# Kernel optimization log

Hardware: AMD Instinct MI355X
Metric: run time of the kernel (lower is better)

The kernel has to match this reference:

```python
import jax, jax.numpy as jnp
import numpy as np

LN_EPS = 1e-5


def _ln(x, g, b):
    mu = jnp.mean(x, -1, keepdims=True)
    xc = x - mu
    inv = jax.lax.rsqrt(jnp.mean(xc * xc, -1, keepdims=True) + LN_EPS)
    return xc * inv * g + b


def _subm_conv(x, nbr, W, b):
    # Submanifold 3D conv via rulebook gather-GEMM-accumulate.
    # x: [N, Cin], nbr: [N, K] neighbor row ids (-1 = missing), W: [K, Cin, Cout], b: [Cout]
    N = x.shape[0]
    xp = jnp.concatenate([x, jnp.zeros((1, x.shape[1]), x.dtype)], 0)  # sentinel zero row
    idx = jnp.where(nbr < 0, N, nbr)  # missing neighbors -> zero row
    acc0 = jnp.zeros((N, W.shape[-1]), x.dtype) + b
    def body(acc, xs):
        i, Wk = xs  # i: [N], Wk: [Cin, Cout]
        return acc + xp[i] @ Wk, None
    acc, _ = jax.lax.scan(body, acc0, (idx.T, W))
    return acc


def _blk1(x, W, b, g, be):  # 1x1x1 SubMConv + LN + ReLU
    return jax.nn.relu(_ln(x @ W + b, g, be))


def _blk3(x, nbr, W, b, g, be):  # 3x3x3 SubMConv + LN + ReLU
    return jax.nn.relu(_ln(_subm_conv(x, nbr, W, b), g, be))


def setup_inputs() -> dict:
    rng = np.random.default_rng(0)
    B, D, Npb, K = 2, 160, 131072, 27
    dim, half = 64, 32
    # Build random sparse voxel set and the rulebook (neighbor table) like spconv does.
    lookup = np.full((B, D, D, D), -1, np.int64)
    coords = np.zeros((B * Npb, 3), np.int64)
    for b in range(B):
        lin = np.sort(rng.choice(D * D * D, size=Npb, replace=False))
        z, y, x = np.unravel_index(lin, (D, D, D))
        rows = np.arange(b * Npb, (b + 1) * Npb)
        lookup[b, z, y, x] = rows
        coords[rows] = np.stack([z, y, x], 1)
    bidx = np.repeat(np.arange(B), Npb)
    offs = np.stack(np.meshgrid(np.arange(-1, 2), np.arange(-1, 2), np.arange(-1, 2), indexing="ij"), -1).reshape(K, 3)
    nz = coords[:, None, :] + offs[None]  # [N, K, 3]
    valid = ((nz >= 0) & (nz < D)).all(-1)
    nzc = np.clip(nz, 0, D - 1)
    nbr = lookup[bidx[:, None], nzc[..., 0], nzc[..., 1], nzc[..., 2]]
    nbr = np.where(valid, nbr, -1).astype(np.int32)

    key = jax.random.key(0)
    ks = iter(jax.random.split(key, 16))
    f32 = jnp.float32
    d = {"voxel_features": jax.random.normal(next(ks), (B * Npb, dim), f32),
         "nbr_idx": jnp.asarray(nbr)}
    def lnp(c):
        return jnp.ones((c,), f32), jnp.zeros((c,), f32)
    d["W1"] = 0.05 * jax.random.normal(next(ks), (dim, dim), f32); d["b1"] = jnp.zeros((dim,), f32); d["g1"], d["be1"] = lnp(dim)
    d["W2"] = 0.05 * jax.random.normal(next(ks), (dim, dim), f32); d["b2"] = jnp.zeros((dim,), f32); d["g2"], d["be2"] = lnp(dim)
    d["W3"] = 0.05 * jax.random.normal(next(ks), (K, dim, half), f32); d["b3"] = jnp.zeros((half,), f32); d["g3"], d["be3"] = lnp(half)
    d["W4"] = 0.05 * jax.random.normal(next(ks), (K, half, half), f32); d["b4"] = jnp.zeros((half,), f32); d["g4"], d["be4"] = lnp(half)
    d["W5"] = 0.05 * jax.random.normal(next(ks), (K, half, half), f32); d["b5"] = jnp.zeros((half,), f32); d["g5"], d["be5"] = lnp(half)
    d["W6"] = 0.05 * jax.random.normal(next(ks), (K, half, half), f32); d["b6"] = jnp.zeros((half,), f32); d["g6"], d["be6"] = lnp(half)
    d["W7"] = 0.05 * jax.random.normal(next(ks), (4 * dim, dim), f32); d["b7"] = jnp.zeros((dim,), f32); d["g7"], d["be7"] = lnp(dim)
    return d


def reference(voxel_features, nbr_idx,
              W1, b1, g1, be1, W2, b2, g2, be2,
              W3, b3, g3, be3, W4, b4, g4, be4,
              W5, b5, g5, be5, W6, b6, g6, be6,
              W7, b7, g7, be7):
    x = voxel_features
    f1 = _blk1(x, W1, b1, g1, be1)
    f2 = _blk1(x, W2, b2, g2, be2)
    feats = [f1, f2]
    f2 = _blk3(f2, nbr_idx, W3, b3, g3, be3); feats.append(f2)
    f2 = _blk3(f2, nbr_idx, W4, b4, g4, be4); feats.append(f2)
    f2 = _blk3(f2, nbr_idx, W5, b5, g5, be5); feats.append(f2)
    f2 = _blk3(f2, nbr_idx, W6, b6, g6, be6); feats.append(f2)
    cat = jnp.concatenate(feats, -1)  # [N, 4*dim]
    return _blk1(cat, W7, b7, g7, be7)
```

## Files before the change

### kernel.cpp

```cpp
#include <hip/hip_runtime.h>

typedef __attribute__((ext_vector_type(4))) float  float4_;
typedef __attribute__((ext_vector_type(8))) short  short8;
typedef __attribute__((ext_vector_type(8))) __bf16 bf16x8;

__device__ inline unsigned short f2bf(float f) {
    unsigned u = __builtin_bit_cast(unsigned, f);
    u += 0x7FFFu + ((u >> 16) & 1u);
    return (unsigned short)(u >> 16);
}

__device__ inline float4_ mfma16(bf16x8 a, bf16x8 b, float4_ c) {
    return __builtin_amdgcn_mfma_f32_16x16x32_bf16(a, b, c, 0, 0, 0);
}

__device__ inline void packW_one(const float* __restrict__ src, unsigned short* __restrict__ dst,
                                 int cin, int cout, int e) {
    int f = e >> 9, i = e & 511, lane = i >> 3, t = i & 7;
    int ntn = cout >> 4, ctn = cin >> 5;
    int nt = f % ntn;
    int rest = f / ntn;
    int ct = rest % ctn;
    int k = rest / ctn;
    int c = ct * 32 + (lane >> 4) * 8 + t;
    int j = nt * 16 + (lane & 15);
    dst[e] = f2bf(src[(k * cin + c) * cout + j]);
}

__global__ void pack_all_kernel(
    const float* __restrict__ W1, const float* __restrict__ W2,
    const float* __restrict__ W3, const float* __restrict__ W4,
    const float* __restrict__ W5, const float* __restrict__ W6,
    const float* __restrict__ W7,
    unsigned short* cat, unsigned short* Wp12, unsigned short* Wp3,
    unsigned short* Wp4, unsigned short* Wp5, unsigned short* Wp6,
    unsigned short* Wp7, int N) {
    int e = blockIdx.x * 256 + threadIdx.x;
    if (e < 8192) {
        int f = e >> 9, i = e & 511, lane = i >> 3, t = i & 7;
        int nt = f & 7, ct = f >> 3;
        int c = ct * 32 + (lane >> 4) * 8 + t;
        int j = nt * 16 + (lane & 15);
        float v = (j < 64) ? W1[c * 64 + j] : W2[c * 64 + (j - 64)];
        Wp12[e] = f2bf(v);
        return;
    }
    e -= 8192;
    if (e < 55296) { packW_one(W3, Wp3, 64, 32, e); return; }
    e -= 55296;
    if (e < 27648) { packW_one(W4, Wp4, 32, 32, e); return; }
    e -= 27648;
    if (e < 27648) { packW_one(W5, Wp5, 32, 32, e); return; }
    e -= 27648;
    if (e < 27648) { packW_one(W6, Wp6, 32, 32, e); return; }
    e -= 27648;
    if (e < 16384) { packW_one(W7, Wp7, 256, 64, e); return; }
    e -= 16384;
    if (e < 128) ((unsigned*)(cat + (size_t)N * 256))[e] = 0;
}

__global__ void nbrT_kernel(const int* __restrict__ nbr, int* __restrict__ nbrT, int N) {
    int row = blockIdx.x * 256 + threadIdx.x;
    if (row >= N) return;
#pragma unroll
    for (int k = 0; k < 27; k++) {
        int v = nbr[(size_t)row * 27 + k];
        nbrT[(size_t)k * N + row] = v < 0 ? N : v;
    }
}

__global__ __launch_bounds__(256) void blk12_kernel(
    const float* __restrict__ x, unsigned short* cat,
    const unsigned short* __restrict__ Wp,
    const float* __restrict__ b1, const float* __restrict__ g1, const float* __restrict__ be1,
    const float* __restrict__ b2, const float* __restrict__ g2, const float* __restrict__ be2) {
    int tid = threadIdx.x, lane = tid & 63, wv = tid >> 6;
    int l15 = lane & 15, q = lane >> 4;
    long base = ((long)blockIdx.x * 4 + wv) * 16;

    float4_ acc[8];
#pragma unroll
    for (int i = 0; i < 8; i++) acc[i] = (float4_){0.f, 0.f, 0.f, 0.f};

#pragma unroll
    for (int kt = 0; kt < 2; kt++) {
        const float* xp = x + (base + l15) * 64 + kt * 32 + q * 8;
        float4_ f0 = *(const float4_*)xp;
        float4_ f1 = *(const float4_*)(xp + 4);
        short8 as;
        as[0] = (short)f2bf(f0[0]); as[1] = (short)f2bf(f0[1]);
        as[2] = (short)f2bf(f0[2]); as[3] = (short)f2bf(f0[3]);
        as[4] = (short)f2bf(f1[0]); as[5] = (short)f2bf(f1[1]);
        as[6] = (short)f2bf(f1[2]); as[7] = (short)f2bf(f1[3]);
        bf16x8 a = __builtin_bit_cast(bf16x8, as);
        const unsigned short* wp = Wp + (size_t)kt * 8 * 512;
#pragma unroll
        for (int nt = 0; nt < 8; nt++) {
            bf16x8 w = *(const bf16x8*)(wp + nt * 512 + lane * 8);
            acc[nt] = mfma16(a, w, acc[nt]);
        }
    }

    float bc[8], gc[8], bec[8];
#pragma unroll
    for (int nt = 0; nt < 8; nt++) {
        int j = nt * 16 + l15;
        if (j < 64) { bc[nt] = b1[j]; gc[nt] = g1[j]; bec[nt] = be1[j]; }
        else        { bc[nt] = b2[j - 64]; gc[nt] = g2[j - 64]; bec[nt] = be2[j - 64]; }
    }

#pragma unroll
    for (int r = 0; r < 4; r++) {
        long row = base + q * 4 + r;
        float v[8], s0 = 0.f, s1 = 0.f, q0 = 0.f, q1 = 0.f;
#pragma unroll
        for (int nt = 0; nt < 4; nt++) { v[nt] = acc[nt][r] + bc[nt]; s0 += v[nt]; q0 += v[nt] * v[nt]; }
#pragma unroll
        for (int nt = 4; nt < 8; nt++) { v[nt] = acc[nt][r] + bc[nt]; s1 += v[nt]; q1 += v[nt] * v[nt]; }
#pragma unroll
        for (int m = 1; m < 16; m <<= 1) {
            s0 += __shfl_xor(s0, m); q0 += __shfl_xor(q0, m);
            s1 += __shfl_xor(s1, m); q1 += __shfl_xor(q1, m);
        }
        float mu0 = s0 * (1.f / 64), var0 = q0 * (1.f / 64) - mu0 * mu0, inv0 = rsqrtf(var0 + 1e-5f);
        float mu1 = s1 * (1.f / 64), var1 = q1 * (1.f / 64) - mu1 * mu1, inv1 = rsqrtf(var1 + 1e-5f);
        unsigned short* cp = cat + row * 256;
#pragma unroll
        for (int nt = 0; nt < 4; nt++) {
            float y = fmaxf((v[nt] - mu0) * inv0 * gc[nt] + bec[nt], 0.f);
            cp[nt * 16 + l15] = f2bf(y);
        }
#pragma unroll
        for (int nt = 4; nt < 8; nt++) {
            float y = fmaxf((v[nt] - mu1) * inv1 * gc[nt] + bec[nt], 0.f);
            cp[nt * 16 + l15] = f2bf(y);
        }
    }
}

template <int CT, int D>
__global__ __launch_bounds__(256) void conv_kernel(
    unsigned short* cat, const int* __restrict__ nbrT,
    const unsigned short* __restrict__ Wp,
    const float* __restrict__ bb, const float* __restrict__ gg, const float* __restrict__ bee,
    int in_off, int out_off, int N) {
    const int MT = 2;
    int tid = threadIdx.x, lane = tid & 63, wv = tid >> 6;
    int l15 = lane & 15, q = lane >> 4;
    int G = gridDim.x;
    int eff = (blockIdx.x & 7) * (G >> 3) + (blockIdx.x >> 3);
    long base = ((long)eff * 4 + wv) * 32;

    float4_ acc[MT][2];
#pragma unroll
    for (int mt = 0; mt < MT; mt++) {
        acc[mt][0] = (float4_){0.f, 0.f, 0.f, 0.f};
        acc[mt][1] = (float4_){0.f, 0.f, 0.f, 0.f};
    }

    const unsigned short* catp = cat + in_off + q * 8;
    const unsigned short* wl = Wp + lane * 8;
    long r0 = base + l15, r1 = base + 16 + l15;

    int    idxr[D + 1][MT];
    bf16x8 f[D + 1][MT][CT];
    bf16x8 wr[D + 1][CT][2];

#pragma unroll
    for (int j = 0; j < D; j++) {
        idxr[j][0] = nbrT[(size_t)j * N + r0];
        idxr[j][1] = nbrT[(size_t)j * N + r1];
    }
#pragma unroll
    for (int j = 0; j < D; j++) {
#pragma unroll
        for (int mt = 0; mt < MT; mt++) {
            size_t s = (size_t)idxr[j % (D + 1)][mt];
#pragma unroll
            for (int ct = 0; ct < CT; ct++)
                f[j % (D + 1)][mt][ct] = *(const bf16x8*)(catp + s * 256 + ct * 32);
        }
#pragma unroll
        for (int ct = 0; ct < CT; ct++)
#pragma unroll
            for (int nt = 0; nt < 2; nt++)
                wr[j % (D + 1)][ct][nt] =
                    *(const bf16x8*)(wl + ((size_t)((j * CT + ct) * 2 + nt)) * 512);
        if (j + D < 27) {
            idxr[(j + D) % (D + 1)][0] = nbrT[(size_t)(j + D) * N + r0];
            idxr[(j + D) % (D + 1)][1] = nbrT[(size_t)(j + D) * N + r1];
        }
    }

#pragma unroll
    for (int k = 0; k < 27; k++) {
        if (k + D < 27) {
#pragma unroll
            for (int mt = 0; mt < MT; mt++) {
                size_t s = (size_t)idxr[(k + D) % (D + 1)][mt];
#pragma unroll
                for (int ct = 0; ct < CT; ct++)
                    f[(k + D) % (D + 1)][mt][ct] = *(const bf16x8*)(catp + s * 256 + ct * 32);
            }
#pragma unroll
            for (int ct = 0; ct < CT; ct++)
#pragma unroll
                for (int nt = 0; nt < 2; nt++)
                    wr[(k + D) % (D + 1)][ct][nt] =
                        *(const bf16x8*)(wl + ((size_t)(((k + D) * CT + ct) * 2 + nt)) * 512);
        }
        if (k + 2 * D < 27) {
            idxr[(k + 2 * D) % (D + 1)][0] = nbrT[(size_t)(k + 2 * D) * N + r0];
            idxr[(k + 2 * D) % (D + 1)][1] = nbrT[(size_t)(k + 2 * D) * N + r1];
        }
        __builtin_amdgcn_sched_barrier(0);
#pragma unroll
        for (int ct = 0; ct < CT; ct++) {
            bf16x8 w0 = wr[k % (D + 1)][ct][0];
            bf16x8 w1 = wr[k % (D + 1)][ct][1];
#pragma unroll
            for (int mt = 0; mt < MT; mt++) {
                acc[mt][0] = mfma16(f[k % (D + 1)][mt][ct], w0, acc[mt][0]);
                acc[mt][1] = mfma16(f[k % (D + 1)][mt][ct], w1, acc[mt][1]);
            }
        }
        __builtin_amdgcn_sched_barrier(0);
    }

    float b0c = bb[l15], b1c = bb[16 + l15];
    float g0c = gg[l15], g1c = gg[16 + l15];
    float be0c = bee[l15], be1c = bee[16 + l15];

#pragma unroll
    for (int mt = 0; mt < MT; mt++) {
#pragma unroll
        for (int r = 0; r < 4; r++) {
            long row = base + mt * 16 + q * 4 + r;
            float v0 = acc[mt][0][r] + b0c;
            float v1 = acc[mt][1][r] + b1c;
            float s = v0 + v1, sq = v0 * v0 + v1 * v1;
#pragma unroll
            for (int m = 1; m < 16; m <<= 1) { s += __shfl_xor(s, m); sq += __shfl_xor(sq, m); }
            float mu = s * (1.f / 32), var = sq * (1.f / 32) - mu * mu, inv = rsqrtf(var + 1e-5f);
            float y0 = fmaxf((v0 - mu) * inv * g0c + be0c, 0.f);
            float y1 = fmaxf((v1 - mu) * inv * g1c + be1c, 0.f);
            unsigned short* cp = cat + row * 256 + out_off;
            cp[l15] = f2bf(y0);
            cp[16 + l15] = f2bf(y1);
        }
    }
}

__global__ __launch_bounds__(256) void blk7_kernel(
    const unsigned short* __restrict__ cat, const unsigned short* __restrict__ Wp,
    const float* __restrict__ b, const float* __restrict__ g, const float* __restrict__ be,
    float* __restrict__ out) {
    int tid = threadIdx.x, lane = tid & 63, wv = tid >> 6;
    int l15 = lane & 15, q = lane >> 4;
    long base = ((long)blockIdx.x * 4 + wv) * 16;

    float4_ acc[4];
#pragma unroll
    for (int i = 0; i < 4; i++) acc[i] = (float4_){0.f, 0.f, 0.f, 0.f};

#pragma unroll
    for (int kt = 0; kt < 8; kt++) {
        bf16x8 a = *(const bf16x8*)(cat + (base + l15) * 256 + kt * 32 + q * 8);
        const unsigned short* wp = Wp + (size_t)kt * 4 * 512;
#pragma unroll
        for (int nt = 0; nt < 4; nt++) {
            bf16x8 w = *(const bf16x8*)(wp + nt * 512 + lane * 8);
            acc[nt] = mfma16(a, w, acc[nt]);
        }
    }

    float bc[4], gc[4], bec[4];
#pragma unroll
    for (int nt = 0; nt < 4; nt++) {
        int j = nt * 16 + l15;
        bc[nt] = b[j]; gc[nt] = g[j]; bec[nt] = be[j];
    }

#pragma unroll
    for (int r = 0; r < 4; r++) {
        long row = base + q * 4 + r;
        float v[4], s = 0.f, sq = 0.f;
#pragma unroll
        for (int nt = 0; nt < 4; nt++) { v[nt] = acc[nt][r] + bc[nt]; s += v[nt]; sq += v[nt] * v[nt]; }
#pragma unroll
        for (int m = 1; m < 16; m <<= 1) { s += __shfl_xor(s, m); sq += __shfl_xor(sq, m); }
        float mu = s * (1.f / 64), var = sq * (1.f / 64) - mu * mu, inv = rsqrtf(var + 1e-5f);
#pragma unroll
        for (int nt = 0; nt < 4; nt++) {
            float y = fmaxf((v[nt] - mu) * inv * gc[nt] + bec[nt], 0.f);
            out[row * 64 + nt * 16 + l15] = y;
        }
    }
}

extern "C" void kernel_launch(void* const* d_in, const int* in_sizes, int n_in,
                              void* d_out, int out_size, void* d_ws, size_t ws_size,
                              hipStream_t stream) {
    const int N = in_sizes[0] / 64;

    const float* x   = (const float*)d_in[0];
    const int*   nbr = (const int*)d_in[1];
    const float* W1 = (const float*)d_in[2];
    const float* b1 = (const float*)d_in[3];
    const float* g1 = (const float*)d_in[4];
    const float* be1 = (const float*)d_in[5];
    const float* W2 = (const float*)d_in[6];
    const float* b2 = (const float*)d_in[7];
    const float* g2 = (const float*)d_in[8];
    const float* be2 = (const float*)d_in[9];
    const float* W3 = (const float*)d_in[10];
    const float* b3 = (const float*)d_in[11];
    const float* g3 = (const float*)d_in[12];
    const float* be3 = (const float*)d_in[13];
    const float* W4 = (const float*)d_in[14];
    const float* b4 = (const float*)d_in[15];
    const float* g4 = (const float*)d_in[16];
    const float* be4 = (const float*)d_in[17];
    const float* W5 = (const float*)d_in[18];
    const float* b5 = (const float*)d_in[19];
    const float* g5 = (const float*)d_in[20];
    const float* be5 = (const float*)d_in[21];
    const float* W6 = (const float*)d_in[22];
    const float* b6 = (const float*)d_in[23];
    const float* g6 = (const float*)d_in[24];
    const float* be6 = (const float*)d_in[25];
    const float* W7 = (const float*)d_in[26];
    const float* b7 = (const float*)d_in[27];
    const float* g7 = (const float*)d_in[28];
    const float* be7 = (const float*)d_in[29];

    unsigned short* ws   = (unsigned short*)d_ws;
    unsigned short* cat  = ws;
    unsigned short* Wp12 = cat + (size_t)(N + 1) * 256;
    unsigned short* Wp3  = Wp12 + 8192;
    unsigned short* Wp4  = Wp3 + 55296;
    unsigned short* Wp5  = Wp4 + 27648;
    unsigned short* Wp6  = Wp5 + 27648;
    unsigned short* Wp7  = Wp6 + 27648;
    int* nbrT = (int*)(Wp7 + 16384);
    nbrT = (int*)(((size_t)nbrT + 15) & ~(size_t)15);

    pack_all_kernel<<<637, 256, 0, stream>>>(W1, W2, W3, W4, W5, W6, W7,
                                             cat, Wp12, Wp3, Wp4, Wp5, Wp6, Wp7, N);
    nbrT_kernel<<<(N + 255) / 256, 256, 0, stream>>>(nbr, nbrT, N);

    blk12_kernel<<<N / 64, 256, 0, stream>>>(x, cat, Wp12, b1, g1, be1, b2, g2, be2);
    conv_kernel<2, 2><<<N / 128, 256, 0, stream>>>(cat, nbrT, Wp3, b3, g3, be3, 64, 128, N);
    conv_kernel<1, 4><<<N / 128, 256, 0, stream>>>(cat, nbrT, Wp4, b4, g4, be4, 128, 160, N);
    conv_kernel<1, 4><<<N / 128, 256, 0, stream>>>(cat, nbrT, Wp5, b5, g5, be5, 160, 192, N);
    conv_kernel<1, 4><<<N / 128, 256, 0, stream>>>(cat, nbrT, Wp6, b6, g6, be6, 192, 224, N);
    blk7_kernel<<<N / 64, 256, 0, stream>>>(cat, Wp7, b7, g7, be7, (float*)d_out);
}
```

Before: 452.1 us.

## Stage neighbor feature window in LDS for subm conv gathers, merge setup kernels

The conv kernel now handles 256 rows per block and splits the 27 offsets into three groups of 9. For each group it computes the min/max neighbor row across the block and copies that contiguous window of input features into shared memory (capped). Gathers then read from LDS, falling back to global memory for neighbors outside the window, with a zero slot for missing ones. This aims to turn scattered global gathers into LDS reads, exploiting the sorted locality of voxels. It adds block-wide syncs, large LDS use that lowers occupancy, and redundant window copies when the index range is wide. Weight packing and neighbor transposition are also merged into one setup launch.

```diff
diff --git a/kernel.cpp b/kernel.cpp
--- a/kernel.cpp
+++ b/kernel.cpp
@@ -8,6 +8,11 @@
     unsigned u = __builtin_bit_cast(unsigned, f);
     u += 0x7FFFu + ((u >> 16) & 1u);
     return (unsigned short)(u >> 16);
+}
+
+__device__ inline bf16x8 zero8() {
+    short8 z = {0, 0, 0, 0, 0, 0, 0, 0};
+    return __builtin_bit_cast(bf16x8, z);
 }
 
 __device__ inline float4_ mfma16(bf16x8 a, bf16x8 b, float4_ c) {
@@ -27,15 +32,29 @@
     dst[e] = f2bf(src[(k * cin + c) * cout + j]);
 }
 
-__global__ void pack_all_kernel(
+#define PACK_TOT 162944
+
+__global__ void setup_kernel(
     const float* __restrict__ W1, const float* __restrict__ W2,
     const float* __restrict__ W3, const float* __restrict__ W4,
     const float* __restrict__ W5, const float* __restrict__ W6,
     const float* __restrict__ W7,
+    const int* __restrict__ nbr, int* __restrict__ nbrT,
     unsigned short* cat, unsigned short* Wp12, unsigned short* Wp3,
     unsigned short* Wp4, unsigned short* Wp5, unsigned short* Wp6,
     unsigned short* Wp7, int N) {
     int e = blockIdx.x * 256 + threadIdx.x;
+    if (e >= PACK_TOT) {
+        int row = e - PACK_TOT;
+        if (row < N) {
+#pragma unroll
+            for (int k = 0; k < 27; k++) {
+                int v = nbr[(size_t)row * 27 + k];
+                nbrT[(size_t)k * N + row] = v < 0 ? N : v;
+            }
+        }
+        return;
+    }
     if (e < 8192) {
         int f = e >> 9, i = e & 511, lane = i >> 3, t = i & 7;
         int nt = f & 7, ct = f >> 3;
@@ -59,16 +78,6 @@
     if (e < 128) ((unsigned*)(cat + (size_t)N * 256))[e] = 0;
 }
 
-__global__ void nbrT_kernel(const int* __restrict__ nbr, int* __restrict__ nbrT, int N) {
-    int row = blockIdx.x * 256 + threadIdx.x;
-    if (row >= N) return;
-#pragma unroll
-    for (int k = 0; k < 27; k++) {
-        int v = nbr[(size_t)row * 27 + k];
-        nbrT[(size_t)k * N + row] = v < 0 ? N : v;
-    }
-}
-
 __global__ __launch_bounds__(256) void blk12_kernel(
     const float* __restrict__ x, unsigned short* cat,
     const unsigned short* __restrict__ Wp,
@@ -138,93 +147,125 @@
     }
 }
 
-template <int CT, int D>
-__global__ __launch_bounds__(256) void conv_kernel(
+template <int CT, int MINW>
+__global__ __launch_bounds__(256, MINW) void conv_kernel(
     unsigned short* cat, const int* __restrict__ nbrT,
     const unsigned short* __restrict__ Wp,
     const float* __restrict__ bb, const float* __restrict__ gg, const float* __restrict__ bee,
     int in_off, int out_off, int N) {
-    const int MT = 2;
+    constexpr int PAY = CT * 32;
+    constexpr int STR = PAY + 8;
+    constexpr int CAP = (CT == 1) ? 500 : 512;
+    constexpr int CHUNKS = PAY / 8;
+    __shared__ __align__(16) unsigned short lds[(CAP + 1) * STR];
+    __shared__ int red[8];
+
     int tid = threadIdx.x, lane = tid & 63, wv = tid >> 6;
     int l15 = lane & 15, q = lane >> 4;
     int G = gridDim.x;
     int eff = (blockIdx.x & 7) * (G >> 3) + (blockIdx.x >> 3);
-    long base = ((long)eff * 4 + wv) * 32;
-
-    float4_ acc[MT][2];
-#pragma unroll
-    for (int mt = 0; mt < MT; mt++) {
+    int wbase = eff * 256 + wv * 64;
+
+    float4_ acc[4][2];
+#pragma unroll
+    for (int mt = 0; mt < 4; mt++) {
         acc[mt][0] = (float4_){0.f, 0.f, 0.f, 0.f};
         acc[mt][1] = (float4_){0.f, 0.f, 0.f, 0.f};
     }
 
-    const unsigned short* catp = cat + in_off + q * 8;
     const unsigned short* wl = Wp + lane * 8;
-    long r0 = base + l15, r1 = base + 16 + l15;
-
-    int    idxr[D + 1][MT];
-    bf16x8 f[D + 1][MT][CT];
-    bf16x8 wr[D + 1][CT][2];
-
-#pragma unroll
-    for (int j = 0; j < D; j++) {
-        idxr[j][0] = nbrT[(size_t)j * N + r0];
-        idxr[j][1] = nbrT[(size_t)j * N + r1];
-    }
-#pragma unroll
-    for (int j = 0; j < D; j++) {
-#pragma unroll
-        for (int mt = 0; mt < MT; mt++) {
-            size_t s = (size_t)idxr[j % (D + 1)][mt];
+
+    if (tid < CHUNKS) *(bf16x8*)(lds + (size_t)CAP * STR + tid * 8) = zero8();
+
+#pragma unroll
+    for (int p = 0; p < 3; p++) {
+        const int kbase = p * 9;
+
+        int idxr[9][4];
+#pragma unroll
+        for (int j = 0; j < 9; j++)
+#pragma unroll
+            for (int mt = 0; mt < 4; mt++)
+                idxr[j][mt] = nbrT[(size_t)(kbase + j) * N + (wbase + mt * 16 + l15)];
+
+        int lmin = 0x7fffffff, lmax = -1;
+#pragma unroll
+        for (int j = 0; j < 9; j++)
+#pragma unroll
+            for (int mt = 0; mt < 4; mt++) {
+                int v = idxr[j][mt];
+                lmin = min(lmin, v == N ? 0x7fffffff : v);
+                lmax = max(lmax, v == N ? -1 : v);
+            }
+#pragma unroll
+        for (int m = 1; m < 64; m <<= 1) {
+            lmin = min(lmin, __shfl_xor(lmin, m));
+            lmax = max(lmax, __shfl_xor(lmax, m));
+        }
+        if (lane == 0) { red[wv] = lmin; red[4 + wv] = lmax; }
+        __syncthreads();
+        int lo = min(min(red[0], red[1]), min(red[2], red[3]));
+        int hi = max(max(red[4], red[5]), max(red[6], red[7]));
+        int cnt = (hi < lo) ? 0 : (hi - lo + 1);
+        if (cnt > CAP) cnt = CAP;
+
+        {
+            int rr = tid / CHUNKS, cc = tid % CHUNKS;
+            for (int r0 = 0; r0 < cnt; r0 += 256 / CHUNKS) {
+                int r = r0 + rr;
+                if (r < cnt)
+                    *(bf16x8*)(lds + (size_t)r * STR + cc * 8) =
+                        *(const bf16x8*)(cat + (size_t)(lo + r) * 256 + in_off + cc * 8);
+            }
+        }
+        __syncthreads();
+
+        bf16x8 fr[3][4][CT];
+        bf16x8 wrr[3][2 * CT];
+
+        auto loadA = [&](int j, int s) {
+#pragma unroll
+            for (int mt = 0; mt < 4; mt++) {
+                int idx = idxr[j][mt];
+                int off = idx - lo;
+                bool inw = (unsigned)off < (unsigned)cnt;
+                int slot = inw ? off : CAP;
+#pragma unroll
+                for (int ct = 0; ct < CT; ct++)
+                    fr[s][mt][ct] = *(const bf16x8*)(lds + (size_t)slot * STR + ct * 32 + q * 8);
+                if (!inw && idx != N) {
+#pragma unroll
+                    for (int ct = 0; ct < CT; ct++)
+                        fr[s][mt][ct] = *(const bf16x8*)(cat + (size_t)idx * 256 + in_off + ct * 32 + q * 8);
+                }
+            }
+        };
+        auto loadW = [&](int k, int s) {
 #pragma unroll
             for (int ct = 0; ct < CT; ct++)
-                f[j % (D + 1)][mt][ct] = *(const bf16x8*)(catp + s * 256 + ct * 32);
-        }
-#pragma unroll
-        for (int ct = 0; ct < CT; ct++)
-#pragma unroll
-            for (int nt = 0; nt < 2; nt++)
-                wr[j % (D + 1)][ct][nt] =
-                    *(const bf16x8*)(wl + ((size_t)((j * CT + ct) * 2 + nt)) * 512);
-        if (j + D < 27) {
-            idxr[(j + D) % (D + 1)][0] = nbrT[(size_t)(j + D) * N + r0];
-            idxr[(j + D) % (D + 1)][1] = nbrT[(size_t)(j + D) * N + r1];
-        }
-    }
-
-#pragma unroll
-    for (int k = 0; k < 27; k++) {
-        if (k + D < 27) {
-#pragma unroll
-            for (int mt = 0; mt < MT; mt++) {
-                size_t s = (size_t)idxr[(k + D) % (D + 1)][mt];
-#pragma unroll
-                for (int ct = 0; ct < CT; ct++)
-                    f[(k + D) % (D + 1)][mt][ct] = *(const bf16x8*)(catp + s * 256 + ct * 32);
-            }
-#pragma unroll
-            for (int ct = 0; ct < CT; ct++)
 #pragma unroll
                 for (int nt = 0; nt < 2; nt++)
-                    wr[(k + D) % (D + 1)][ct][nt] =
-                        *(const bf16x8*)(wl + ((size_t)(((k + D) * CT + ct) * 2 + nt)) * 512);
-        }
-        if (k + 2 * D < 27) {
-            idxr[(k + 2 * D) % (D + 1)][0] = nbrT[(size_t)(k + 2 * D) * N + r0];
-            idxr[(k + 2 * D) % (D + 1)][1] = nbrT[(size_t)(k + 2 * D) * N + r1];
-        }
-        __builtin_amdgcn_sched_barrier(0);
-#pragma unroll
-        for (int ct = 0; ct < CT; ct++) {
-            bf16x8 w0 = wr[k % (D + 1)][ct][0];
-            bf16x8 w1 = wr[k % (D + 1)][ct][1];
-#pragma unroll
-            for (int mt = 0; mt < MT; mt++) {
-                acc[mt][0] = mfma16(f[k % (D + 1)][mt][ct], w0, acc[mt][0]);
-                acc[mt][1] = mfma16(f[k % (D + 1)][mt][ct], w1, acc[mt][1]);
-            }
-        }
-        __builtin_amdgcn_sched_barrier(0);
+                    wrr[s][ct * 2 + nt] =
+                        *(const bf16x8*)(wl + ((size_t)((k * CT + ct) * 2 + nt)) * 512);
+        };
+
+        loadA(0, 0); loadW(kbase + 0, 0);
+        loadA(1, 1); loadW(kbase + 1, 1);
+#pragma unroll
+        for (int j = 0; j < 9; j++) {
+            if (j + 2 < 9) { loadA(j + 2, (j + 2) % 3); loadW(kbase + j + 2, (j + 2) % 3); }
+            int s = j % 3;
+#pragma unroll
+            for (int ct = 0; ct < CT; ct++) {
+                bf16x8 w0 = wrr[s][ct * 2];
+                bf16x8 w1 = wrr[s][ct * 2 + 1];
+#pragma unroll
+                for (int mt = 0; mt < 4; mt++) {
+                    acc[mt][0] = mfma16(fr[s][mt][ct], w0, acc[mt][0]);
+                    acc[mt][1] = mfma16(fr[s][mt][ct], w1, acc[mt][1]);
+                }
+            }
+        }
     }
 
     float b0c = bb[l15], b1c = bb[16 + l15];
@@ -232,10 +273,10 @@
     float be0c = bee[l15], be1c = bee[16 + l15];
 
 #pragma unroll
-    for (int mt = 0; mt < MT; mt++) {
+    for (int mt = 0; mt < 4; mt++) {
 #pragma unroll
         for (int r = 0; r < 4; r++) {
-            long row = base + mt * 16 + q * 4 + r;
+            long row = (long)wbase + mt * 16 + q * 4 + r;
             float v0 = acc[mt][0][r] + b0c;
             float v1 = acc[mt][1][r] + b1c;
             float s = v0 + v1, sq = v0 * v0 + v1 * v1;
@@ -345,14 +386,14 @@
     int* nbrT = (int*)(Wp7 + 16384);
     nbrT = (int*)(((size_t)nbrT + 15) & ~(size_t)15);
 
-    pack_all_kernel<<<637, 256, 0, stream>>>(W1, W2, W3, W4, W5, W6, W7,
-                                             cat, Wp12, Wp3, Wp4, Wp5, Wp6, Wp7, N);
-    nbrT_kernel<<<(N + 255) / 256, 256, 0, stream>>>(nbr, nbrT, N);
+    int setup_blocks = (PACK_TOT + N + 255) / 256;
+    setup_kernel<<<setup_blocks, 256, 0, stream>>>(W1, W2, W3, W4, W5, W6, W7,
+                                                   nbr, nbrT, cat, Wp12, Wp3, Wp4, Wp5, Wp6, Wp7, N);
 
     blk12_kernel<<<N / 64, 256, 0, stream>>>(x, cat, Wp12, b1, g1, be1, b2, g2, be2);
-    conv_kernel<2, 2><<<N / 128, 256, 0, stream>>>(cat, nbrT, Wp3, b3, g3, be3, 64, 128, N);
-    conv_kernel<1, 4><<<N / 128, 256, 0, stream>>>(cat, nbrT, Wp4, b4, g4, be4, 128, 160, N);
-    conv_kernel<1, 4><<<N / 128, 256, 0, stream>>>(cat, nbrT, Wp5, b5, g5, be5, 160, 192, N);
-    conv_kernel<1, 4><<<N / 128, 256, 0, stream>>>(cat, nbrT, Wp6, b6, g6, be6, 192, 224, N);
+    conv_kernel<2, 2><<<N / 256, 256, 0, stream>>>(cat, nbrT, Wp3, b3, g3, be3, 64, 128, N);
+    conv_kernel<1, 3><<<N / 256, 256, 0, stream>>>(cat, nbrT, Wp4, b4, g4, be4, 128, 160, N);
+    conv_kernel<1, 3><<<N / 256, 256, 0, stream>>>(cat, nbrT, Wp5, b5, g5, be5, 160, 192, N);
+    conv_kernel<1, 3><<<N / 256, 256, 0, stream>>>(cat, nbrT, Wp6, b6, g6, be6, 192, 224, N);
     blk7_kernel<<<N / 64, 256, 0, stream>>>(cat, Wp7, b7, g7, be7, (float*)d_out);
 }
```

Result: slower. 463.4 us (+2.5%).

## Split conv reduction over taps across waves with LDS reduction; fuse setup kernels

Applied to the files above, without the earlier changes.

Restructures the submanifold conv kernel so the four waves of a block each take a slice of the 27×Cin tap units for the same small row tile, issuing all their gathers up front, then reduce partial accumulators through shared memory before bias+LayerNorm+ReLU with vectorized bf16 stores. This trades per-wave row parallelism for split-K parallelism, aiming to expose more independent gathers in flight and raise occupancy (launch bounds 3), at the cost of an LDS round trip and barrier. It also merges the weight-pack and neighbor-transpose kernels into one launch to save a launch.

```diff
diff --git a/kernel.cpp b/kernel.cpp
--- a/kernel.cpp
+++ b/kernel.cpp
@@ -3,6 +3,8 @@
 typedef __attribute__((ext_vector_type(4))) float  float4_;
 typedef __attribute__((ext_vector_type(8))) short  short8;
 typedef __attribute__((ext_vector_type(8))) __bf16 bf16x8;
+typedef __attribute__((ext_vector_type(4))) unsigned short u16x4;
+typedef __attribute__((ext_vector_type(2))) unsigned short u16x2;
 
 __device__ inline unsigned short f2bf(float f) {
     unsigned u = __builtin_bit_cast(unsigned, f);
@@ -27,15 +29,29 @@
     dst[e] = f2bf(src[(k * cin + c) * cout + j]);
 }
 
-__global__ void pack_all_kernel(
+#define PACK_TOT 162944
+
+__global__ void setup_kernel(
     const float* __restrict__ W1, const float* __restrict__ W2,
     const float* __restrict__ W3, const float* __restrict__ W4,
     const float* __restrict__ W5, const float* __restrict__ W6,
     const float* __restrict__ W7,
+    const int* __restrict__ nbr, int* __restrict__ nbrT,
     unsigned short* cat, unsigned short* Wp12, unsigned short* Wp3,
     unsigned short* Wp4, unsigned short* Wp5, unsigned short* Wp6,
     unsigned short* Wp7, int N) {
     int e = blockIdx.x * 256 + threadIdx.x;
+    if (e >= PACK_TOT) {
+        int row = e - PACK_TOT;
+        if (row < N) {
+#pragma unroll
+            for (int k = 0; k < 27; k++) {
+                int v = nbr[(size_t)row * 27 + k];
+                nbrT[(size_t)k * N + row] = v < 0 ? N : v;
+            }
+        }
+        return;
+    }
     if (e < 8192) {
         int f = e >> 9, i = e & 511, lane = i >> 3, t = i & 7;
         int nt = f & 7, ct = f >> 3;
@@ -59,16 +75,6 @@
     if (e < 128) ((unsigned*)(cat + (size_t)N * 256))[e] = 0;
 }
 
-__global__ void nbrT_kernel(const int* __restrict__ nbr, int* __restrict__ nbrT, int N) {
-    int row = blockIdx.x * 256 + threadIdx.x;
-    if (row >= N) return;
-#pragma unroll
-    for (int k = 0; k < 27; k++) {
-        int v = nbr[(size_t)row * 27 + k];
-        nbrT[(size_t)k * N + row] = v < 0 ? N : v;
-    }
-}
-
 __global__ __launch_bounds__(256) void blk12_kernel(
     const float* __restrict__ x, unsigned short* cat,
     const unsigned short* __restrict__ Wp,
@@ -138,18 +144,52 @@
     }
 }
 
-template <int CT, int D>
-__global__ __launch_bounds__(256) void conv_kernel(
+template <int CIN_T, int MT>
+__global__ __launch_bounds__(256, 3) void conv_kernel(
     unsigned short* cat, const int* __restrict__ nbrT,
     const unsigned short* __restrict__ Wp,
     const float* __restrict__ bb, const float* __restrict__ gg, const float* __restrict__ bee,
     int in_off, int out_off, int N) {
-    const int MT = 2;
-    int tid = threadIdx.x, lane = tid & 63, wv = tid >> 6;
+    constexpr int UNITS = 27 * CIN_T;
+    constexpr int UMAX  = (UNITS + 3) / 4;
+    constexpr int ROWS  = MT * 16;
+    constexpr int TPR   = 256 / ROWS;
+    constexpr int CPT   = 32 / TPR;
+
+    __shared__ float plds[4][ROWS][33];
+
+    int tid = threadIdx.x, lane = tid & 63, w = tid >> 6;
     int l15 = lane & 15, q = lane >> 4;
     int G = gridDim.x;
     int eff = (blockIdx.x & 7) * (G >> 3) + (blockIdx.x >> 3);
-    long base = ((long)eff * 4 + wv) * 32;
+    long base = (long)eff * ROWS;
+
+    int u0 = (w * UNITS) / 4;
+    int nu = ((w + 1) * UNITS) / 4 - u0;
+
+    int sidx[UMAX][MT];
+#pragma unroll
+    for (int j = 0; j < UMAX; j++) {
+        int uc  = (u0 + j < UNITS) ? u0 + j : UNITS - 1;
+        int tap = uc / CIN_T;
+        bool act = j < nu;
+#pragma unroll
+        for (int mt = 0; mt < MT; mt++) {
+            int v = nbrT[(size_t)tap * N + base + mt * 16 + l15];
+            sidx[j][mt] = act ? v : N;
+        }
+    }
+
+    bf16x8 f[UMAX][MT];
+#pragma unroll
+    for (int j = 0; j < UMAX; j++) {
+        int uc = (u0 + j < UNITS) ? u0 + j : UNITS - 1;
+        int ct = uc % CIN_T;
+        const unsigned short* cp = cat + in_off + ct * 32 + q * 8;
+#pragma unroll
+        for (int mt = 0; mt < MT; mt++)
+            f[j][mt] = *(const bf16x8*)(cp + (size_t)sidx[j][mt] * 256);
+    }
 
     float4_ acc[MT][2];
 #pragma unroll
@@ -157,97 +197,50 @@
         acc[mt][0] = (float4_){0.f, 0.f, 0.f, 0.f};
         acc[mt][1] = (float4_){0.f, 0.f, 0.f, 0.f};
     }
-
-    const unsigned short* catp = cat + in_off + q * 8;
-    const unsigned short* wl = Wp + lane * 8;
-    long r0 = base + l15, r1 = base + 16 + l15;
-
-    int    idxr[D + 1][MT];
-    bf16x8 f[D + 1][MT][CT];
-    bf16x8 wr[D + 1][CT][2];
-
-#pragma unroll
-    for (int j = 0; j < D; j++) {
-        idxr[j][0] = nbrT[(size_t)j * N + r0];
-        idxr[j][1] = nbrT[(size_t)j * N + r1];
-    }
-#pragma unroll
-    for (int j = 0; j < D; j++) {
+#pragma unroll
+    for (int j = 0; j < UMAX; j++) {
+        int uc = (u0 + j < UNITS) ? u0 + j : UNITS - 1;
+        const unsigned short* wp = Wp + (size_t)uc * 1024 + lane * 8;
+        bf16x8 w0 = *(const bf16x8*)(wp);
+        bf16x8 w1 = *(const bf16x8*)(wp + 512);
 #pragma unroll
         for (int mt = 0; mt < MT; mt++) {
-            size_t s = (size_t)idxr[j % (D + 1)][mt];
-#pragma unroll
-            for (int ct = 0; ct < CT; ct++)
-                f[j % (D + 1)][mt][ct] = *(const bf16x8*)(catp + s * 256 + ct * 32);
-        }
-#pragma unroll
-        for (int ct = 0; ct < CT; ct++)
-#pragma unroll
-            for (int nt = 0; nt < 2; nt++)
-                wr[j % (D + 1)][ct][nt] =
-                    *(const bf16x8*)(wl + ((size_t)((j * CT + ct) * 2 + nt)) * 512);
-        if (j + D < 27) {
-            idxr[(j + D) % (D + 1)][0] = nbrT[(size_t)(j + D) * N + r0];
-            idxr[(j + D) % (D + 1)][1] = nbrT[(size_t)(j + D) * N + r1];
-        }
-    }
-
-#pragma unroll
-    for (int k = 0; k < 27; k++) {
-        if (k + D < 27) {
-#pragma unroll
-            for (int mt = 0; mt < MT; mt++) {
-                size_t s = (size_t)idxr[(k + D) % (D + 1)][mt];
-#pragma unroll
-                for (int ct = 0; ct < CT; ct++)
-                    f[(k + D) % (D + 1)][mt][ct] = *(const bf16x8*)(catp + s * 256 + ct * 32);
-            }
-#pragma unroll
-            for (int ct = 0; ct < CT; ct++)
-#pragma unroll
-                for (int nt = 0; nt < 2; nt++)
-                    wr[(k + D) % (D + 1)][ct][nt] =
-                        *(const bf16x8*)(wl + ((size_t)(((k + D) * CT + ct) * 2 + nt)) * 512);
-        }
-        if (k + 2 * D < 27) {
-            idxr[(k + 2 * D) % (D + 1)][0] = nbrT[(size_t)(k + 2 * D) * N + r0];
-            idxr[(k + 2 * D) % (D + 1)][1] = nbrT[(size_t)(k + 2 * D) * N + r1];
-        }
-        __builtin_amdgcn_sched_barrier(0);
-#pragma unroll
-        for (int ct = 0; ct < CT; ct++) {
-            bf16x8 w0 = wr[k % (D + 1)][ct][0];
-            bf16x8 w1 = wr[k % (D + 1)][ct][1];
-#pragma unroll
-            for (int mt = 0; mt < MT; mt++) {
-                acc[mt][0] = mfma16(f[k % (D + 1)][mt][ct], w0, acc[mt][0]);
-                acc[mt][1] = mfma16(f[k % (D + 1)][mt][ct], w1, acc[mt][1]);
-            }
-        }
-        __builtin_amdgcn_sched_barrier(0);
-    }
-
-    float b0c = bb[l15], b1c = bb[16 + l15];
-    float g0c = gg[l15], g1c = gg[16 + l15];
-    float be0c = bee[l15], be1c = bee[16 + l15];
-
-#pragma unroll
-    for (int mt = 0; mt < MT; mt++) {
+            acc[mt][0] = mfma16(f[j][mt], w0, acc[mt][0]);
+            acc[mt][1] = mfma16(f[j][mt], w1, acc[mt][1]);
+        }
+    }
+
+#pragma unroll
+    for (int mt = 0; mt < MT; mt++)
 #pragma unroll
         for (int r = 0; r < 4; r++) {
-            long row = base + mt * 16 + q * 4 + r;
-            float v0 = acc[mt][0][r] + b0c;
-            float v1 = acc[mt][1][r] + b1c;
-            float s = v0 + v1, sq = v0 * v0 + v1 * v1;
-#pragma unroll
-            for (int m = 1; m < 16; m <<= 1) { s += __shfl_xor(s, m); sq += __shfl_xor(sq, m); }
-            float mu = s * (1.f / 32), var = sq * (1.f / 32) - mu * mu, inv = rsqrtf(var + 1e-5f);
-            float y0 = fmaxf((v0 - mu) * inv * g0c + be0c, 0.f);
-            float y1 = fmaxf((v1 - mu) * inv * g1c + be1c, 0.f);
-            unsigned short* cp = cat + row * 256 + out_off;
-            cp[l15] = f2bf(y0);
-            cp[16 + l15] = f2bf(y1);
-        }
+            plds[w][mt * 16 + q * 4 + r][l15]      = acc[mt][0][r];
+            plds[w][mt * 16 + q * 4 + r][16 + l15] = acc[mt][1][r];
+        }
+    __syncthreads();
+
+    int row = tid / TPR;
+    int cs  = (tid % TPR) * CPT;
+    float v[CPT], s = 0.f, sq = 0.f;
+#pragma unroll
+    for (int c = 0; c < CPT; c++) {
+        float t = bb[cs + c];
+#pragma unroll
+        for (int ww = 0; ww < 4; ww++) t += plds[ww][row][cs + c];
+        v[c] = t; s += t; sq += t * t;
+    }
+#pragma unroll
+    for (int m = 1; m < TPR; m <<= 1) { s += __shfl_xor(s, m); sq += __shfl_xor(sq, m); }
+    float mu = s * (1.f / 32), var = sq * (1.f / 32) - mu * mu, inv = rsqrtf(var + 1e-5f);
+    unsigned short ov[CPT];
+#pragma unroll
+    for (int c = 0; c < CPT; c++)
+        ov[c] = f2bf(fmaxf((v[c] - mu) * inv * gg[cs + c] + bee[cs + c], 0.f));
+    unsigned short* dst = cat + (base + row) * 256 + out_off + cs;
+    if constexpr (CPT == 4) {
+        *(u16x4*)dst = (u16x4){ov[0], ov[1], ov[2], ov[3]};
+    } else {
+        *(u16x2*)dst = (u16x2){ov[0], ov[1]};
     }
 }
 
@@ -345,14 +338,14 @@
     int* nbrT = (int*)(Wp7 + 16384);
     nbrT = (int*)(((size_t)nbrT + 15) & ~(size_t)15);
 
-    pack_all_kernel<<<637, 256, 0, stream>>>(W1, W2, W3, W4, W5, W6, W7,
-                                             cat, Wp12, Wp3, Wp4, Wp5, Wp6, Wp7, N);
-    nbrT_kernel<<<(N + 255) / 256, 256, 0, stream>>>(nbr, nbrT, N);
+    int setup_blocks = (PACK_TOT + N + 255) / 256;
+    setup_kernel<<<setup_blocks, 256, 0, stream>>>(W1, W2, W3, W4, W5, W6, W7,
+                                                   nbr, nbrT, cat, Wp12, Wp3, Wp4, Wp5, Wp6, Wp7, N);
 
     blk12_kernel<<<N / 64, 256, 0, stream>>>(x, cat, Wp12, b1, g1, be1, b2, g2, be2);
-    conv_kernel<2, 2><<<N / 128, 256, 0, stream>>>(cat, nbrT, Wp3, b3, g3, be3, 64, 128, N);
-    conv_kernel<1, 4><<<N / 128, 256, 0, stream>>>(cat, nbrT, Wp4, b4, g4, be4, 128, 160, N);
-    conv_kernel<1, 4><<<N / 128, 256, 0, stream>>>(cat, nbrT, Wp5, b5, g5, be5, 160, 192, N);
-    conv_kernel<1, 4><<<N / 128, 256, 0, stream>>>(cat, nbrT, Wp6, b6, g6, be6, 192, 224, N);
+    conv_kernel<2, 1><<<N / 16, 256, 0, stream>>>(cat, nbrT, Wp3, b3, g3, be3, 64, 128, N);
+    conv_kernel<1, 2><<<N / 32, 256, 0, stream>>>(cat, nbrT, Wp4, b4, g4, be4, 128, 160, N);
+    conv_kernel<1, 2><<<N / 32, 256, 0, stream>>>(cat, nbrT, Wp5, b5, g5, be5, 160, 192, N);
+    conv_kernel<1, 2><<<N / 32, 256, 0, stream>>>(cat, nbrT, Wp6, b6, g6, be6, 192, 224, N);
     blk7_kernel<<<N / 64, 256, 0, stream>>>(cat, Wp7, b7, g7, be7, (float*)d_out);
 }
```

After: 482.3 us. 1.07x slower.

## Widen conv row tiles, switch to double-buffered gathers, merge setup kernels

Applied to the files above, without the earlier changes.

The conv kernel is now templated on rows per wave (MT), raised to 4 for the 64-channel conv and 8 for the 32-channel convs, so each weight fragment load feeds more MFMAs. The deep D-stage prefetch ring becomes a simple two-slot double buffer, the sched barriers are removed, and launch bounds are set to 2 blocks per CU. The weight-pack and neighbor-transpose kernels are merged into one setup launch. In exchange, grids shrink to 1024 or 512 blocks, which lowers parallelism and the number of gathers in flight per wave, and that may hurt latency hiding for the random row gathers.

```diff
diff --git a/kernel.cpp b/kernel.cpp
--- a/kernel.cpp
+++ b/kernel.cpp
@@ -27,15 +27,29 @@
     dst[e] = f2bf(src[(k * cin + c) * cout + j]);
 }
 
-__global__ void pack_all_kernel(
+#define PACK_TOT 162944
+
+__global__ void setup_kernel(
     const float* __restrict__ W1, const float* __restrict__ W2,
     const float* __restrict__ W3, const float* __restrict__ W4,
     const float* __restrict__ W5, const float* __restrict__ W6,
     const float* __restrict__ W7,
+    const int* __restrict__ nbr, int* __restrict__ nbrT,
     unsigned short* cat, unsigned short* Wp12, unsigned short* Wp3,
     unsigned short* Wp4, unsigned short* Wp5, unsigned short* Wp6,
     unsigned short* Wp7, int N) {
     int e = blockIdx.x * 256 + threadIdx.x;
+    if (e >= PACK_TOT) {
+        int row = e - PACK_TOT;
+        if (row < N) {
+#pragma unroll
+            for (int k = 0; k < 27; k++) {
+                int v = nbr[(size_t)row * 27 + k];
+                nbrT[(size_t)k * N + row] = v < 0 ? N : v;
+            }
+        }
+        return;
+    }
     if (e < 8192) {
         int f = e >> 9, i = e & 511, lane = i >> 3, t = i & 7;
         int nt = f & 7, ct = f >> 3;
@@ -59,16 +73,6 @@
     if (e < 128) ((unsigned*)(cat + (size_t)N * 256))[e] = 0;
 }
 
-__global__ void nbrT_kernel(const int* __restrict__ nbr, int* __restrict__ nbrT, int N) {
-    int row = blockIdx.x * 256 + threadIdx.x;
-    if (row >= N) return;
-#pragma unroll
-    for (int k = 0; k < 27; k++) {
-        int v = nbr[(size_t)row * 27 + k];
-        nbrT[(size_t)k * N + row] = v < 0 ? N : v;
-    }
-}
-
 __global__ __launch_bounds__(256) void blk12_kernel(
     const float* __restrict__ x, unsigned short* cat,
     const unsigned short* __restrict__ Wp,
@@ -138,18 +142,17 @@
     }
 }
 
-template <int CT, int D>
-__global__ __launch_bounds__(256) void conv_kernel(
+template <int CT, int MT>
+__global__ __launch_bounds__(256, 2) void conv_kernel(
     unsigned short* cat, const int* __restrict__ nbrT,
     const unsigned short* __restrict__ Wp,
     const float* __restrict__ bb, const float* __restrict__ gg, const float* __restrict__ bee,
     int in_off, int out_off, int N) {
-    const int MT = 2;
     int tid = threadIdx.x, lane = tid & 63, wv = tid >> 6;
     int l15 = lane & 15, q = lane >> 4;
     int G = gridDim.x;
     int eff = (blockIdx.x & 7) * (G >> 3) + (blockIdx.x >> 3);
-    long base = ((long)eff * 4 + wv) * 32;
+    long base = ((long)eff * 4 + wv) * (MT * 16);
 
     float4_ acc[MT][2];
 #pragma unroll
@@ -160,71 +163,60 @@
 
     const unsigned short* catp = cat + in_off + q * 8;
     const unsigned short* wl = Wp + lane * 8;
-    long r0 = base + l15, r1 = base + 16 + l15;
-
-    int    idxr[D + 1][MT];
-    bf16x8 f[D + 1][MT][CT];
-    bf16x8 wr[D + 1][CT][2];
-
-#pragma unroll
-    for (int j = 0; j < D; j++) {
-        idxr[j][0] = nbrT[(size_t)j * N + r0];
-        idxr[j][1] = nbrT[(size_t)j * N + r1];
-    }
-#pragma unroll
-    for (int j = 0; j < D; j++) {
-#pragma unroll
-        for (int mt = 0; mt < MT; mt++) {
-            size_t s = (size_t)idxr[j % (D + 1)][mt];
-#pragma unroll
-            for (int ct = 0; ct < CT; ct++)
-                f[j % (D + 1)][mt][ct] = *(const bf16x8*)(catp + s * 256 + ct * 32);
-        }
+
+    int    idxs[2][MT];
+    bf16x8 fr[2][MT][CT];
+    bf16x8 wr[2][CT][2];
+
+#pragma unroll
+    for (int mt = 0; mt < MT; mt++) idxs[0][mt] = nbrT[base + mt * 16 + l15];
+#pragma unroll
+    for (int mt = 0; mt < MT; mt++) {
+        size_t s = (size_t)idxs[0][mt] * 256;
 #pragma unroll
         for (int ct = 0; ct < CT; ct++)
-#pragma unroll
-            for (int nt = 0; nt < 2; nt++)
-                wr[j % (D + 1)][ct][nt] =
-                    *(const bf16x8*)(wl + ((size_t)((j * CT + ct) * 2 + nt)) * 512);
-        if (j + D < 27) {
-            idxr[(j + D) % (D + 1)][0] = nbrT[(size_t)(j + D) * N + r0];
-            idxr[(j + D) % (D + 1)][1] = nbrT[(size_t)(j + D) * N + r1];
-        }
-    }
+            fr[0][mt][ct] = *(const bf16x8*)(catp + s + ct * 32);
+    }
+#pragma unroll
+    for (int ct = 0; ct < CT; ct++) {
+        wr[0][ct][0] = *(const bf16x8*)(wl + (size_t)(ct * 2) * 512);
+        wr[0][ct][1] = *(const bf16x8*)(wl + (size_t)(ct * 2 + 1) * 512);
+    }
+#pragma unroll
+    for (int mt = 0; mt < MT; mt++) idxs[1][mt] = nbrT[(size_t)N + base + mt * 16 + l15];
 
 #pragma unroll
     for (int k = 0; k < 27; k++) {
-        if (k + D < 27) {
+        const int cur = k & 1, nxt = cur ^ 1;
+        if (k + 1 < 27) {
 #pragma unroll
             for (int mt = 0; mt < MT; mt++) {
-                size_t s = (size_t)idxr[(k + D) % (D + 1)][mt];
+                size_t s = (size_t)idxs[nxt][mt] * 256;
 #pragma unroll
                 for (int ct = 0; ct < CT; ct++)
-                    f[(k + D) % (D + 1)][mt][ct] = *(const bf16x8*)(catp + s * 256 + ct * 32);
+                    fr[nxt][mt][ct] = *(const bf16x8*)(catp + s + ct * 32);
             }
 #pragma unroll
-            for (int ct = 0; ct < CT; ct++)
-#pragma unroll
-                for (int nt = 0; nt < 2; nt++)
-                    wr[(k + D) % (D + 1)][ct][nt] =
-                        *(const bf16x8*)(wl + ((size_t)(((k + D) * CT + ct) * 2 + nt)) * 512);
-        }
-        if (k + 2 * D < 27) {
-            idxr[(k + 2 * D) % (D + 1)][0] = nbrT[(size_t)(k + 2 * D) * N + r0];
-            idxr[(k + 2 * D) % (D + 1)][1] = nbrT[(size_t)(k + 2 * D) * N + r1];
-        }
-        __builtin_amdgcn_sched_barrier(0);
+            for (int ct = 0; ct < CT; ct++) {
+                wr[nxt][ct][0] = *(const bf16x8*)(wl + (size_t)(((k + 1) * CT + ct) * 2) * 512);
+                wr[nxt][ct][1] = *(const bf16x8*)(wl + (size_t)(((k + 1) * CT + ct) * 2 + 1) * 512);
+            }
+        }
+        if (k + 2 < 27) {
+#pragma unroll
+            for (int mt = 0; mt < MT; mt++)
+                idxs[cur][mt] = nbrT[(size_t)(k + 2) * N + base + mt * 16 + l15];
+        }
 #pragma unroll
         for (int ct = 0; ct < CT; ct++) {
-            bf16x8 w0 = wr[k % (D + 1)][ct][0];
-            bf16x8 w1 = wr[k % (D + 1)][ct][1];
+            bf16x8 w0 = wr[cur][ct][0];
+            bf16x8 w1 = wr[cur][ct][1];
 #pragma unroll
             for (int mt = 0; mt < MT; mt++) {
-                acc[mt][0] = mfma16(f[k % (D + 1)][mt][ct], w0, acc[mt][0]);
-                acc[mt][1] = mfma16(f[k % (D + 1)][mt][ct], w1, acc[mt][1]);
+                acc[mt][0] = mfma16(fr[cur][mt][ct], w0, acc[mt][0]);
+                acc[mt][1] = mfma16(fr[cur][mt][ct], w1, acc[mt][1]);
             }
         }
-        __builtin_amdgcn_sched_barrier(0);
     }
 
     float b0c = bb[l15], b1c = bb[16 + l15];
@@ -345,14 +337,14 @@
     int* nbrT = (int*)(Wp7 + 16384);
     nbrT = (int*)(((size_t)nbrT + 15) & ~(size_t)15);
 
-    pack_all_kernel<<<637, 256, 0, stream>>>(W1, W2, W3, W4, W5, W6, W7,
-                                             cat, Wp12, Wp3, Wp4, Wp5, Wp6, Wp7, N);
-    nbrT_kernel<<<(N + 255) / 256, 256, 0, stream>>>(nbr, nbrT, N);
+    int setup_blocks = (PACK_TOT + N + 255) / 256;
+    setup_kernel<<<setup_blocks, 256, 0, stream>>>(W1, W2, W3, W4, W5, W6, W7,
+                                                   nbr, nbrT, cat, Wp12, Wp3, Wp4, Wp5, Wp6, Wp7, N);
 
     blk12_kernel<<<N / 64, 256, 0, stream>>>(x, cat, Wp12, b1, g1, be1, b2, g2, be2);
-    conv_kernel<2, 2><<<N / 128, 256, 0, stream>>>(cat, nbrT, Wp3, b3, g3, be3, 64, 128, N);
-    conv_kernel<1, 4><<<N / 128, 256, 0, stream>>>(cat, nbrT, Wp4, b4, g4, be4, 128, 160, N);
-    conv_kernel<1, 4><<<N / 128, 256, 0, stream>>>(cat, nbrT, Wp5, b5, g5, be5, 160, 192, N);
-    conv_kernel<1, 4><<<N / 128, 256, 0, stream>>>(cat, nbrT, Wp6, b6, g6, be6, 192, 224, N);
+    conv_kernel<2, 4><<<N / 256, 256, 0, stream>>>(cat, nbrT, Wp3, b3, g3, be3, 64, 128, N);
+    conv_kernel<1, 8><<<N / 512, 256, 0, stream>>>(cat, nbrT, Wp4, b4, g4, be4, 128, 160, N);
+    conv_kernel<1, 8><<<N / 512, 256, 0, stream>>>(cat, nbrT, Wp5, b5, g5, be5, 160, 192, N);
+    conv_kernel<1, 8><<<N / 512, 256, 0, stream>>>(cat, nbrT, Wp6, b6, g6, be6, 192, 224, N);
     blk7_kernel<<<N / 64, 256, 0, stream>>>(cat, Wp7, b7, g7, be7, (float*)d_out);
 }
```

Result: slower. 475.5 us (+5.2%).
